# Kernel tuning notes

Hardware: AMD Instinct MI355X
Metric: run time of the kernel (lower is better)

Reference implementation:

```python
import jax, jax.numpy as jnp
import numpy as np

N, H, E, A, T = 50000, 128, 800000, 16, 4


def setup_inputs() -> dict:
    key = jax.random.key(0)
    ks = jax.random.split(key, 12)
    s = 1.0 / np.sqrt(H + A)
    s2 = 1.0 / np.sqrt(H)
    return {
        "h": jax.random.normal(ks[0], (N, H), dtype=jnp.float32),
        "edge_index": jax.random.randint(ks[1], (2, E), 0, N, dtype=jnp.int32),
        "edge_type": jax.random.randint(ks[2], (E,), 0, T, dtype=jnp.int32),
        "edge_attr": jax.random.normal(ks[3], (E, A), dtype=jnp.float32),
        # per-edge-type 2-layer MLP params
        "W1": jax.random.uniform(ks[4], (T, H + A, H), minval=-s, maxval=s, dtype=jnp.float32),
        "b1": jax.random.uniform(ks[5], (T, H), minval=-s, maxval=s, dtype=jnp.float32),
        "W2": jax.random.uniform(ks[6], (T, H, H), minval=-s2, maxval=s2, dtype=jnp.float32),
        "b2": jax.random.uniform(ks[7], (T, H), minval=-s2, maxval=s2, dtype=jnp.float32),
        # GRUCell params (torch layout: [3H, H] with gate order r, z, n)
        "w_ih": jax.random.uniform(ks[8], (3 * H, H), minval=-s2, maxval=s2, dtype=jnp.float32),
        "w_hh": jax.random.uniform(ks[9], (3 * H, H), minval=-s2, maxval=s2, dtype=jnp.float32),
        "b_ih": jax.random.uniform(ks[10], (3 * H,), minval=-s2, maxval=s2, dtype=jnp.float32),
        "b_hh": jax.random.uniform(ks[11], (3 * H,), minval=-s2, maxval=s2, dtype=jnp.float32),
    }


def reference(h, edge_index, edge_type, edge_attr, W1, b1, W2, b2, w_ih, w_hh, b_ih, b_hh):
    src, dst = edge_index[0], edge_index[1]
    h_in = jnp.concatenate([h[src], edge_attr], axis=-1)  # [E, H+A]
    # per-edge-type MLP; loop over small fixed num_edge_types, mask-select
    m = jnp.zeros((h_in.shape[0], H), dtype=h.dtype)
    for t in range(T):
        mt = jax.nn.relu(h_in @ W1[t] + b1[t]) @ W2[t] + b2[t]  # [E, H]
        m = jnp.where((edge_type == t)[:, None], mt, m)
    # scatter-add messages to destination nodes
    msg = jax.ops.segment_sum(m, dst, num_segments=h.shape[0])  # [N, H]
    # GRUCell(msg, h) with torch gate order r, z, n
    gi = msg @ w_ih.T + b_ih  # [N, 3H]
    gh = h @ w_hh.T + b_hh
    i_r, i_z, i_n = jnp.split(gi, 3, axis=-1)
    h_r, h_z, h_n = jnp.split(gh, 3, axis=-1)
    r = jax.nn.sigmoid(i_r + h_r)
    z = jax.nn.sigmoid(i_z + h_z)
    n = jnp.tanh(i_n + r * h_n)
    return (1.0 - z) * n + z * h
```

## Files before the change

kernel.cpp:

```cpp
#include <hip/hip_runtime.h>
#include <stdint.h>

#define Hh 128
#define Aa 16
#define Tt 4
#define K1 144
#define W1T_LD 168
#define WG_LD  136
#define YT_LD  136

typedef float f32x4 __attribute__((ext_vector_type(4)));
typedef __bf16 bf16x8 __attribute__((ext_vector_type(8)));
typedef unsigned short u16x8 __attribute__((ext_vector_type(8)));
typedef unsigned short u16x4 __attribute__((ext_vector_type(4)));
typedef unsigned short u16x2 __attribute__((ext_vector_type(2)));

static __device__ __forceinline__ unsigned short f2bf(float f) {
    unsigned u = __builtin_bit_cast(unsigned, f);
    u += 0x7fffu + ((u >> 16) & 1u);
    return (unsigned short)(u >> 16);
}

static __device__ __forceinline__ float bf2f(unsigned short u) {
    return __builtin_bit_cast(float, (unsigned)u << 16);
}

static __device__ __forceinline__ bf16x8 pack8(const float* __restrict__ x) {
    f32x4 a = *(const f32x4*)x;
    f32x4 b = *(const f32x4*)(x + 4);
    u16x8 t;
    t[0] = f2bf(a[0]); t[1] = f2bf(a[1]); t[2] = f2bf(a[2]); t[3] = f2bf(a[3]);
    t[4] = f2bf(b[0]); t[5] = f2bf(b[1]); t[6] = f2bf(b[2]); t[7] = f2bf(b[3]);
    return __builtin_bit_cast(bf16x8, t);
}

static __device__ __forceinline__ bf16x8 zero_bf8() {
    u16x8 z = {0, 0, 0, 0, 0, 0, 0, 0};
    return __builtin_bit_cast(bf16x8, z);
}

__global__ void cast_kernel(const float* __restrict__ src, unsigned short* __restrict__ dst, int n4) {
    int i = blockIdx.x * blockDim.x + threadIdx.x;
    if (i < n4) {
        f32x4 v = *(const f32x4*)(src + (size_t)i * 4);
        u16x4 o;
        o[0] = f2bf(v[0]); o[1] = f2bf(v[1]); o[2] = f2bf(v[2]); o[3] = f2bf(v[3]);
        *(u16x4*)(dst + (size_t)i * 4) = o;
    }
}

__global__ void hist_kernel(const int* __restrict__ et, const int* __restrict__ eidx,
                            int E, int N, int* __restrict__ cnt, unsigned* __restrict__ rank) {
    for (int i = blockIdx.x * blockDim.x + threadIdx.x; i < E; i += gridDim.x * blockDim.x) {
        int tt = et[i];
        unsigned rD = (unsigned)atomicAdd(&cnt[tt * N + eidx[E + i]], 1);
        unsigned rS = (unsigned)atomicAdd(&cnt[4 * N + tt * N + eidx[i]], 1);
        rank[i] = rD | (rS << 16);
    }
}

__global__ void scanA_kernel(const int* __restrict__ deg2, int nb, int* __restrict__ bsum) {
    __shared__ int red[256];
    const int t = threadIdx.x;
    const int i0 = blockIdx.x * 1024 + t * 4;
    int s = 0;
    #pragma unroll
    for (int j = 0; j < 4; j++) if (i0 + j < nb) s += deg2[i0 + j];
    red[t] = s; __syncthreads();
    for (int d = 128; d > 0; d >>= 1) {
        if (t < d) red[t] += red[t + d];
        __syncthreads();
    }
    if (t == 0) bsum[blockIdx.x] = red[0];
}

__global__ void scanB_kernel(int* __restrict__ bsum, int nblocks,
                             int* __restrict__ rowptrD, int fourN, int E) {
    __shared__ int ts[512];
    const int t = threadIdx.x;
    int v = (t < nblocks) ? bsum[t] : 0;
    ts[t] = v; __syncthreads();
    for (int d = 1; d < 512; d <<= 1) {
        int x = (t >= d) ? ts[t - d] : 0;
        __syncthreads();
        ts[t] += x;
        __syncthreads();
    }
    if (t < nblocks) bsum[t] = ts[t] - v;
    if (t == 0) rowptrD[fourN] = E;
}

__global__ void scanC_kernel(int* __restrict__ cur, int nb, int fourN,
                             const int* __restrict__ bsum, int* __restrict__ rowptrD) {
    __shared__ int ts[256];
    const int t = threadIdx.x;
    const int i0 = blockIdx.x * 1024 + t * 4;
    int v[4];
    #pragma unroll
    for (int j = 0; j < 4; j++) v[j] = (i0 + j < nb) ? cur[i0 + j] : 0;
    int s = v[0] + v[1] + v[2] + v[3];
    ts[t] = s; __syncthreads();
    for (int d = 1; d < 256; d <<= 1) {
        int x = (t >= d) ? ts[t - d] : 0;
        __syncthreads();
        ts[t] += x;
        __syncthreads();
    }
    int run = bsum[blockIdx.x] + ts[t] - s;
    #pragma unroll
    for (int j = 0; j < 4; j++) {
        if (i0 + j < nb) {
            if (i0 + j < fourN) rowptrD[i0 + j] = run;
            cur[i0 + j] = run;
            run += v[j];
        }
    }
}

__global__ void fill2_kernel(const int* __restrict__ et, const int* __restrict__ eidx,
                             int E, int N, const int* __restrict__ binstart,
                             const unsigned* __restrict__ rank, int4* __restrict__ rec) {
    for (int i = blockIdx.x * blockDim.x + threadIdx.x; i < E; i += gridDim.x * blockDim.x) {
        int tt = et[i];
        int d = eidx[E + i], s = eidx[i];
        unsigned r = rank[i];
        int posD = binstart[tt * N + d] + (int)(r & 0xffffu);
        int posS = binstart[4 * N + tt * N + s] + (int)(r >> 16) - E;
        rec[posS] = make_int4(s, i, posD, 0);
    }
}

__global__ __launch_bounds__(512) void l1_kernel(
    const unsigned short* __restrict__ h_bf, const int4* __restrict__ rec,
    const float* __restrict__ eattr, const unsigned short* __restrict__ W1bf,
    const float* __restrict__ b1, const int* __restrict__ rowptrD,
    unsigned short* __restrict__ Yg, int N)
{
    __shared__ unsigned short W1T[128 * W1T_LD];
    __shared__ float b1s[128];
    __shared__ unsigned short yt[8 * 8 * YT_LD];
    const int t = blockIdx.x & 3;
    const int lb = blockIdx.x >> 2;
    const int nbk = gridDim.x >> 2;
    const int tid = threadIdx.x;

    for (int idx = tid; idx < K1 * Hh; idx += 512) {
        int k = idx >> 7, n = idx & 127;
        W1T[n * W1T_LD + k] = W1bf[((size_t)t * K1 + k) * Hh + n];
    }
    for (int idx = tid; idx < (W1T_LD - K1) * Hh; idx += 512) {
        int k = K1 + (idx % (W1T_LD - K1)), n = idx / (W1T_LD - K1);
        W1T[n * W1T_LD + k] = 0;
    }
    if (tid < 128) b1s[tid] = b1[t * Hh + tid];
    __syncthreads();

    const int tstart = rowptrD[t * N];
    const int tend = rowptrD[(t + 1) * N];
    const int cnt = tend - tstart;
    const int ntiles = (cnt + 255) >> 8;
    const int w = tid >> 6, lane = tid & 63;
    const int l15 = lane & 15, q = lane >> 4;
    unsigned short* __restrict__ ytw = yt + w * 8 * YT_LD;

    for (int tile = lb; tile < ntiles; tile += nbk) {
        const int p0 = tstart + tile * 256 + w * 32;
        const int pa = p0 + l15, pb = p0 + 16 + l15;
        const bool va = pa < tend, vb = pb < tend;
        const int4 ra = rec[va ? pa : tstart];
        const int4 rb = rec[vb ? pb : tstart];
        const int sa = ra.x, sb = rb.x;
        const int ea = ra.y, eb = rb.y;
        const int ypa = ra.z, ypb = rb.z;
        const unsigned short* __restrict__ hA = h_bf + (size_t)sa * Hh;
        const unsigned short* __restrict__ hB = h_bf + (size_t)sb * Hh;

        f32x4 acc[8][2];
        #pragma unroll
        for (int mt = 0; mt < 8; mt++) {
            acc[mt][0] = (f32x4){0.f, 0.f, 0.f, 0.f};
            acc[mt][1] = (f32x4){0.f, 0.f, 0.f, 0.f};
        }

        #pragma unroll
        for (int ks = 0; ks < 5; ks++) {
            const int k0 = ks * 32;
            bf16x8 fb_a, fb_b;
            if (ks < 4) {
                fb_a = __builtin_bit_cast(bf16x8, *(const u16x8*)(hA + k0 + q * 8));
                fb_b = __builtin_bit_cast(bf16x8, *(const u16x8*)(hB + k0 + q * 8));
            } else if (q < 2) {
                fb_a = pack8(eattr + (size_t)ea * Aa + q * 8);
                fb_b = pack8(eattr + (size_t)eb * Aa + q * 8);
            } else {
                fb_a = zero_bf8();
                fb_b = zero_bf8();
            }
            #pragma unroll
            for (int mt = 0; mt < 8; mt++) {
                bf16x8 fa = *(const bf16x8*)&W1T[(mt * 16 + l15) * W1T_LD + k0 + q * 8];
                acc[mt][0] = __builtin_amdgcn_mfma_f32_16x16x32_bf16(fa, fb_a, acc[mt][0], 0, 0, 0);
                acc[mt][1] = __builtin_amdgcn_mfma_f32_16x16x32_bf16(fa, fb_b, acc[mt][1], 0, 0, 0);
            }
        }

        #pragma unroll
        for (int g = 0; g < 2; g++) {
            const int yp = g ? ypb : ypa;
            #pragma unroll
            for (int s = 0; s < 2; s++) {
                if ((l15 >> 3) == s) {
                    #pragma unroll
                    for (int mt = 0; mt < 8; mt++) {
                        f32x4 bias = *(const f32x4*)&b1s[mt * 16 + q * 4];
                        u16x4 y;
                        #pragma unroll
                        for (int i = 0; i < 4; i++) {
                            float v = acc[mt][g][i] + bias[i];
                            y[i] = f2bf(v > 0.f ? v : 0.f);
                        }
                        *(u16x4*)&ytw[(l15 & 7) * YT_LD + mt * 16 + q * 4] = y;
                    }
                }
                __asm__ volatile("s_waitcnt lgkmcnt(0)" ::: "memory");
                #pragma unroll
                for (int r0 = 0; r0 < 2; r0++) {
                    const int el = r0 * 4 + q;
                    if (p0 + g * 16 + s * 8 + el < tend) {
                        const int yrow = __shfl(yp, s * 8 + el);
                        u16x8 v = *(const u16x8*)&ytw[el * YT_LD + l15 * 8];
                        *(u16x8*)&Yg[(size_t)yrow * Hh + l15 * 8] = v;
                    }
                }
                __asm__ volatile("s_waitcnt lgkmcnt(0)" ::: "memory");
            }
        }
    }
}

__global__ __launch_bounds__(256) void zgemm_kernel(
    const unsigned short* __restrict__ Yg, const int* __restrict__ rowptrD,
    const unsigned short* __restrict__ W2bf, const float* __restrict__ b2,
    unsigned short* __restrict__ msgb, int N)
{
    __shared__ unsigned short W2T[128 * WG_LD];
    __shared__ float b2s[512];
    __shared__ int cntS[4 * 64];
    const int tid = threadIdx.x;
    const int w = tid >> 6, lane = tid & 63;
    const int l15 = lane & 15, q = lane >> 4;
    const int nodebase = blockIdx.x * 64 + w * 16;
    const int nA = min(nodebase + l15, N - 1);

    if (tid < 512) {
        b2s[tid] = b2[tid];
        b2s[tid + 256] = b2[tid + 256];
    }

    f32x4 acc[8];
    #pragma unroll
    for (int ct = 0; ct < 8; ct++) acc[ct] = (f32x4){0.f, 0.f, 0.f, 0.f};

    for (int t = 0; t < Tt; t++) {
        __syncthreads();
        for (int idx = tid; idx < Hh * Hh; idx += 256) {
            int k = idx >> 7, n = idx & 127;
            W2T[n * WG_LD + k] = W2bf[((size_t)t * Hh + k) * Hh + n];
        }
        __syncthreads();

        const int seg = rowptrD[(size_t)t * N + nA];
        const int len = rowptrD[(size_t)t * N + nA + 1] - seg;
        cntS[w * 64 + t * 16 + l15] = len;

        float asum[32];
        #pragma unroll
        for (int i = 0; i < 32; i++) asum[i] = 0.f;
        for (int j = 0; j < len; j++) {
            const unsigned short* __restrict__ yr = Yg + (size_t)(seg + j) * Hh;
            #pragma unroll
            for (int ks = 0; ks < 4; ks++) {
                u16x8 yv = *(const u16x8*)(yr + ks * 32 + q * 8);
                #pragma unroll
                for (int e = 0; e < 8; e++) asum[ks * 8 + e] += bf2f(yv[e]);
            }
        }

        #pragma unroll
        for (int ks = 0; ks < 4; ks++) {
            u16x8 fr;
            #pragma unroll
            for (int e = 0; e < 8; e++) fr[e] = f2bf(asum[ks * 8 + e]);
            bf16x8 fa = __builtin_bit_cast(bf16x8, fr);
            #pragma unroll
            for (int ct = 0; ct < 8; ct++) {
                bf16x8 fb = *(const bf16x8*)&W2T[(ct * 16 + l15) * WG_LD + ks * 32 + q * 8];
                acc[ct] = __builtin_amdgcn_mfma_f32_16x16x32_bf16(fa, fb, acc[ct], 0, 0, 0);
            }
        }
    }
    __syncthreads();

    #pragma unroll
    for (int ct = 0; ct < 8; ct++) {
        const int c = ct * 16 + l15;
        #pragma unroll
        for (int i = 0; i < 4; i++) {
            int node = nodebase + q * 4 + i;
            if (node < N) {
                float bias = 0.f;
                #pragma unroll
                for (int t = 0; t < Tt; t++)
                    bias += (float)cntS[w * 64 + t * 16 + q * 4 + i] * b2s[t * 128 + c];
                msgb[(size_t)node * Hh + c] = f2bf(acc[ct][i] + bias);
            }
        }
    }
}

__global__ __launch_bounds__(512) void gru_kernel(
    const float* __restrict__ h, const unsigned short* __restrict__ msgb,
    const unsigned short* __restrict__ wihb, const unsigned short* __restrict__ whhb,
    const float* __restrict__ b_ih, const float* __restrict__ b_hh,
    float* __restrict__ out, int N)
{
    __shared__ unsigned short Wg[128 * WG_LD];
    const int tid = threadIdx.x;
    const int w = tid >> 6, lane = tid & 63;
    const int l15 = lane & 15, q = lane >> 4;
    const int nodebase = blockIdx.x * 128 + w * 16;
    const int nA = min(nodebase + l15, N - 1);
    const unsigned short* __restrict__ mrow = msgb + (size_t)nA * Hh;
    const float* __restrict__ hrow = h + (size_t)nA * Hh;

    f32x4 gr[8], gz[8], gin[8], ghn[8];
    #pragma unroll
    for (int ct = 0; ct < 8; ct++) {
        gr[ct] = (f32x4){0.f, 0.f, 0.f, 0.f};
        gz[ct] = (f32x4){0.f, 0.f, 0.f, 0.f};
        gin[ct] = (f32x4){0.f, 0.f, 0.f, 0.f};
        ghn[ct] = (f32x4){0.f, 0.f, 0.f, 0.f};
    }

    auto stage = [&](const unsigned short* __restrict__ Ws, int gate) {
        __syncthreads();
        for (int idx = tid; idx < Hh * Hh / 2; idx += 512) {
            int o = idx >> 6, kk = (idx & 63) * 2;
            *(u16x2*)&Wg[o * WG_LD + kk] =
                *(const u16x2*)&Ws[(size_t)gate * Hh * Hh + o * Hh + kk];
        }
        __syncthreads();
    };
    auto matmulM = [&](f32x4* acc) {
        #pragma unroll
        for (int ks = 0; ks < 4; ks++) {
            bf16x8 fa = __builtin_bit_cast(bf16x8, *(const u16x8*)(mrow + ks * 32 + q * 8));
            #pragma unroll
            for (int ct = 0; ct < 8; ct++) {
                bf16x8 fb = *(const bf16x8*)&Wg[(ct * 16 + l15) * WG_LD + ks * 32 + q * 8];
                acc[ct] = __builtin_amdgcn_mfma_f32_16x16x32_bf16(fa, fb, acc[ct], 0, 0, 0);
            }
        }
    };
    auto matmulH = [&](f32x4* acc) {
        #pragma unroll
        for (int ks = 0; ks < 4; ks++) {
            bf16x8 fa = pack8(hrow + ks * 32 + q * 8);
            #pragma unroll
            for (int ct = 0; ct < 8; ct++) {
                bf16x8 fb = *(const bf16x8*)&Wg[(ct * 16 + l15) * WG_LD + ks * 32 + q * 8];
                acc[ct] = __builtin_amdgcn_mfma_f32_16x16x32_bf16(fa, fb, acc[ct], 0, 0, 0);
            }
        }
    };

    stage(wihb, 0); matmulM(gr);
    stage(whhb, 0); matmulH(gr);
    stage(wihb, 1); matmulM(gz);
    stage(whhb, 1); matmulH(gz);
    stage(wihb, 2); matmulM(gin);
    stage(whhb, 2); matmulH(ghn);

    #pragma unroll
    for (int ct = 0; ct < 8; ct++) {
        int c = ct * 16 + l15;
        float bir = b_ih[c],       bhr = b_hh[c];
        float biz = b_ih[128 + c], bhz = b_hh[128 + c];
        float bin = b_ih[256 + c], bhn = b_hh[256 + c];
        #pragma unroll
        for (int i = 0; i < 4; i++) {
            int node = nodebase + q * 4 + i;
            if (node < N) {
                float rv = 1.f / (1.f + __expf(-(gr[ct][i] + bir + bhr)));
                float zv = 1.f / (1.f + __expf(-(gz[ct][i] + biz + bhz)));
                float npre = gin[ct][i] + bin + rv * (ghn[ct][i] + bhn);
                float e2 = __expf(-2.f * npre);
                float nv = (1.f - e2) / (1.f + e2);
                float hv = h[(size_t)node * Hh + c];
                out[(size_t)node * Hh + c] = (1.f - zv) * nv + zv * hv;
            }
        }
    }
}

static inline size_t align256(size_t x) { return (x + 255) & ~(size_t)255; }

extern "C" void kernel_launch(void* const* d_in, const int* in_sizes, int n_in,
                              void* d_out, int out_size, void* d_ws, size_t ws_size,
                              hipStream_t stream)
{
    const float* h     = (const float*)d_in[0];
    const int*   eidx  = (const int*)d_in[1];
    const int*   et    = (const int*)d_in[2];
    const float* eattr = (const float*)d_in[3];
    const float* W1    = (const float*)d_in[4];
    const float* b1    = (const float*)d_in[5];
    const float* W2    = (const float*)d_in[6];
    const float* b2    = (const float*)d_in[7];
    const float* w_ih  = (const float*)d_in[8];
    const float* w_hh  = (const float*)d_in[9];
    const float* b_ih  = (const float*)d_in[10];
    const float* b_hh  = (const float*)d_in[11];

    const int N = in_sizes[0] / Hh;
    const int E = in_sizes[1] / 2;
    const int nb = 8 * N;
    const int sblocks = (nb + 1023) / 1024;

    char* p = (char*)d_ws;
    unsigned short* msgb = (unsigned short*)p; p += align256((size_t)N * Hh * sizeof(unsigned short));
    unsigned short* Yg = (unsigned short*)p;   p += align256((size_t)E * Hh * sizeof(unsigned short));
    int4* rec = (int4*)p;               p += align256((size_t)E * sizeof(int4));
    unsigned* rank = (unsigned*)p;      p += align256((size_t)E * sizeof(unsigned));
    int* rowptrD = (int*)p;             p += align256(((size_t)4 * N + 1) * sizeof(int));
    int* cur = (int*)p;                 p += align256((size_t)nb * sizeof(int));
    int* bsum = (int*)p;                p += align256(1024 * sizeof(int));
    unsigned short* h_bf = (unsigned short*)p; p += align256((size_t)N * Hh * sizeof(unsigned short));
    unsigned short* W1bf = (unsigned short*)p; p += align256((size_t)Tt * K1 * Hh * sizeof(unsigned short));
    unsigned short* W2bf = (unsigned short*)p; p += align256((size_t)Tt * Hh * Hh * sizeof(unsigned short));
    unsigned short* wihb = (unsigned short*)p; p += align256((size_t)3 * Hh * Hh * sizeof(unsigned short));
    unsigned short* whhb = (unsigned short*)p; p += align256((size_t)3 * Hh * Hh * sizeof(unsigned short));

    hipMemsetAsync(cur, 0, (size_t)nb * sizeof(int), stream);

    {
        int n4h = N * Hh / 4, n41 = Tt * K1 * Hh / 4, n42 = Tt * Hh * Hh / 4;
        int n4g = 3 * Hh * Hh / 4;
        cast_kernel<<<(n4h + 255) / 256, 256, 0, stream>>>(h, h_bf, n4h);
        cast_kernel<<<(n41 + 255) / 256, 256, 0, stream>>>(W1, W1bf, n41);
        cast_kernel<<<(n42 + 255) / 256, 256, 0, stream>>>(W2, W2bf, n42);
        cast_kernel<<<(n4g + 255) / 256, 256, 0, stream>>>(w_ih, wihb, n4g);
        cast_kernel<<<(n4g + 255) / 256, 256, 0, stream>>>(w_hh, whhb, n4g);
    }

    hist_kernel<<<1024, 256, 0, stream>>>(et, eidx, E, N, cur, rank);
    scanA_kernel<<<sblocks, 256, 0, stream>>>(cur, nb, bsum);
    scanB_kernel<<<1, 512, 0, stream>>>(bsum, sblocks, rowptrD, 4 * N, E);
    scanC_kernel<<<sblocks, 256, 0, stream>>>(cur, nb, 4 * N, bsum, rowptrD);
    fill2_kernel<<<1024, 256, 0, stream>>>(et, eidx, E, N, cur, rank, rec);

    l1_kernel<<<1024, 512, 0, stream>>>(h_bf, rec, eattr, W1bf, b1, rowptrD, Yg, N);
    zgemm_kernel<<<(N + 63) / 64, 256, 0, stream>>>(Yg, rowptrD, W2bf, b2, msgb, N);

    int gblocks = (N + 127) / 128;
    gru_kernel<<<gblocks, 512, 0, stream>>>(h, msgb, wihb, whhb, b_ih, b_hh, (float*)d_out, N);
}
```

Measured before the change: 491.0 us.

## Merge cast launches, drop LDS staging in l1 epilogue, preload GRU fragments

Merges the five bf16 cast launches into a single kernel. In the layer-1 kernel, the output is written straight to global memory from the MFMA accumulators instead of being staged through shared memory with shuffles, and the W1 transpose load is vectorized. The kernel also gets an occupancy hint, and the grid size is doubled. The GRU kernel now preloads msg and h fragments once (reading the bf16 copy of h) and reuses them across the six gate matmuls, with wider weight staging loads. The direct l1 stores are narrower 8-byte scattered writes, which may coalesce less well than the old 16-byte row stores.

```diff
diff --git a/kernel.cpp b/kernel.cpp
--- a/kernel.cpp
+++ b/kernel.cpp
@@ -7,7 +7,6 @@
 #define K1 144
 #define W1T_LD 168
 #define WG_LD  136
-#define YT_LD  136
 
 typedef float f32x4 __attribute__((ext_vector_type(4)));
 typedef __bf16 bf16x8 __attribute__((ext_vector_type(8)));
@@ -39,14 +38,27 @@
     return __builtin_bit_cast(bf16x8, z);
 }
 
-__global__ void cast_kernel(const float* __restrict__ src, unsigned short* __restrict__ dst, int n4) {
+__global__ void cast_all_kernel(
+    const float* __restrict__ h, const float* __restrict__ W1,
+    const float* __restrict__ W2, const float* __restrict__ wih,
+    const float* __restrict__ whh,
+    unsigned short* __restrict__ h_bf, unsigned short* __restrict__ W1bf,
+    unsigned short* __restrict__ W2bf, unsigned short* __restrict__ wihb,
+    unsigned short* __restrict__ whhb,
+    int n0, int n1, int n2, int n3, int n4)
+{
     int i = blockIdx.x * blockDim.x + threadIdx.x;
-    if (i < n4) {
-        f32x4 v = *(const f32x4*)(src + (size_t)i * 4);
-        u16x4 o;
-        o[0] = f2bf(v[0]); o[1] = f2bf(v[1]); o[2] = f2bf(v[2]); o[3] = f2bf(v[3]);
-        *(u16x4*)(dst + (size_t)i * 4) = o;
-    }
+    if (i >= n4) return;
+    const float* s; unsigned short* d; int off;
+    if (i < n0)      { s = h;   d = h_bf; off = i; }
+    else if (i < n1) { s = W1;  d = W1bf; off = i - n0; }
+    else if (i < n2) { s = W2;  d = W2bf; off = i - n1; }
+    else if (i < n3) { s = wih; d = wihb; off = i - n2; }
+    else             { s = whh; d = whhb; off = i - n3; }
+    f32x4 v = *(const f32x4*)(s + (size_t)off * 4);
+    u16x4 o;
+    o[0] = f2bf(v[0]); o[1] = f2bf(v[1]); o[2] = f2bf(v[2]); o[3] = f2bf(v[3]);
+    *(u16x4*)(d + (size_t)off * 4) = o;
 }
 
 __global__ void hist_kernel(const int* __restrict__ et, const int* __restrict__ eidx,
@@ -130,7 +142,7 @@
     }
 }
 
-__global__ __launch_bounds__(512) void l1_kernel(
+__global__ __launch_bounds__(512, 6) void l1_kernel(
     const unsigned short* __restrict__ h_bf, const int4* __restrict__ rec,
     const float* __restrict__ eattr, const unsigned short* __restrict__ W1bf,
     const float* __restrict__ b1, const int* __restrict__ rowptrD,
@@ -138,19 +150,21 @@
 {
     __shared__ unsigned short W1T[128 * W1T_LD];
     __shared__ float b1s[128];
-    __shared__ unsigned short yt[8 * 8 * YT_LD];
     const int t = blockIdx.x & 3;
     const int lb = blockIdx.x >> 2;
     const int nbk = gridDim.x >> 2;
     const int tid = threadIdx.x;
 
-    for (int idx = tid; idx < K1 * Hh; idx += 512) {
-        int k = idx >> 7, n = idx & 127;
-        W1T[n * W1T_LD + k] = W1bf[((size_t)t * K1 + k) * Hh + n];
-    }
-    for (int idx = tid; idx < (W1T_LD - K1) * Hh; idx += 512) {
-        int k = K1 + (idx % (W1T_LD - K1)), n = idx / (W1T_LD - K1);
-        W1T[n * W1T_LD + k] = 0;
+    for (int idx = tid; idx < (K1 * Hh) / 8; idx += 512) {
+        int k = idx >> 4, n0 = (idx & 15) * 8;
+        u16x8 v = *(const u16x8*)&W1bf[((size_t)t * K1 + k) * Hh + n0];
+        #pragma unroll
+        for (int j = 0; j < 8; j++) W1T[(n0 + j) * W1T_LD + k] = v[j];
+    }
+    for (int idx = tid; idx < Hh * 3; idx += 512) {
+        int n = idx / 3, c = (idx % 3) * 8;
+        u16x8 z = {0, 0, 0, 0, 0, 0, 0, 0};
+        *(u16x8*)&W1T[n * W1T_LD + K1 + c] = z;
     }
     if (tid < 128) b1s[tid] = b1[t * Hh + tid];
     __syncthreads();
@@ -161,7 +175,6 @@
     const int ntiles = (cnt + 255) >> 8;
     const int w = tid >> 6, lane = tid & 63;
     const int l15 = lane & 15, q = lane >> 4;
-    unsigned short* __restrict__ ytw = yt + w * 8 * YT_LD;
 
     for (int tile = lb; tile < ntiles; tile += nbk) {
         const int p0 = tstart + tile * 256 + w * 32;
@@ -206,33 +219,19 @@
 
         #pragma unroll
         for (int g = 0; g < 2; g++) {
-            const int yp = g ? ypb : ypa;
-            #pragma unroll
-            for (int s = 0; s < 2; s++) {
-                if ((l15 >> 3) == s) {
+            if (g ? vb : va) {
+                unsigned short* __restrict__ o = Yg + (size_t)(g ? ypb : ypa) * Hh + q * 4;
+                #pragma unroll
+                for (int mt = 0; mt < 8; mt++) {
+                    f32x4 bias = *(const f32x4*)&b1s[mt * 16 + q * 4];
+                    u16x4 y;
                     #pragma unroll
-                    for (int mt = 0; mt < 8; mt++) {
-                        f32x4 bias = *(const f32x4*)&b1s[mt * 16 + q * 4];
-                        u16x4 y;
-                        #pragma unroll
-                        for (int i = 0; i < 4; i++) {
-                            float v = acc[mt][g][i] + bias[i];
-                            y[i] = f2bf(v > 0.f ? v : 0.f);
-                        }
-                        *(u16x4*)&ytw[(l15 & 7) * YT_LD + mt * 16 + q * 4] = y;
+                    for (int i = 0; i < 4; i++) {
+                        float v = acc[mt][g][i] + bias[i];
+                        y[i] = f2bf(v > 0.f ? v : 0.f);
                     }
+                    *(u16x4*)(o + mt * 16) = y;
                 }
-                __asm__ volatile("s_waitcnt lgkmcnt(0)" ::: "memory");
-                #pragma unroll
-                for (int r0 = 0; r0 < 2; r0++) {
-                    const int el = r0 * 4 + q;
-                    if (p0 + g * 16 + s * 8 + el < tend) {
-                        const int yrow = __shfl(yp, s * 8 + el);
-                        u16x8 v = *(const u16x8*)&ytw[el * YT_LD + l15 * 8];
-                        *(u16x8*)&Yg[(size_t)yrow * Hh + l15 * 8] = v;
-                    }
-                }
-                __asm__ volatile("s_waitcnt lgkmcnt(0)" ::: "memory");
             }
         }
     }
@@ -319,7 +318,8 @@
 }
 
 __global__ __launch_bounds__(512) void gru_kernel(
-    const float* __restrict__ h, const unsigned short* __restrict__ msgb,
+    const float* __restrict__ h, const unsigned short* __restrict__ h_bf,
+    const unsigned short* __restrict__ msgb,
     const unsigned short* __restrict__ wihb, const unsigned short* __restrict__ whhb,
     const float* __restrict__ b_ih, const float* __restrict__ b_hh,
     float* __restrict__ out, int N)
@@ -330,8 +330,13 @@
     const int l15 = lane & 15, q = lane >> 4;
     const int nodebase = blockIdx.x * 128 + w * 16;
     const int nA = min(nodebase + l15, N - 1);
-    const unsigned short* __restrict__ mrow = msgb + (size_t)nA * Hh;
-    const float* __restrict__ hrow = h + (size_t)nA * Hh;
+
+    bf16x8 fm[4], fh[4];
+    #pragma unroll
+    for (int ks = 0; ks < 4; ks++) {
+        fm[ks] = __builtin_bit_cast(bf16x8, *(const u16x8*)(msgb + (size_t)nA * Hh + ks * 32 + q * 8));
+        fh[ks] = __builtin_bit_cast(bf16x8, *(const u16x8*)(h_bf + (size_t)nA * Hh + ks * 32 + q * 8));
+    }
 
     f32x4 gr[8], gz[8], gin[8], ghn[8];
     #pragma unroll
@@ -344,42 +349,30 @@
 
     auto stage = [&](const unsigned short* __restrict__ Ws, int gate) {
         __syncthreads();
-        for (int idx = tid; idx < Hh * Hh / 2; idx += 512) {
-            int o = idx >> 6, kk = (idx & 63) * 2;
-            *(u16x2*)&Wg[o * WG_LD + kk] =
-                *(const u16x2*)&Ws[(size_t)gate * Hh * Hh + o * Hh + kk];
+        for (int idx = tid; idx < (Hh * Hh) / 8; idx += 512) {
+            int o = idx >> 4, k8 = (idx & 15) * 8;
+            *(u16x8*)&Wg[o * WG_LD + k8] =
+                *(const u16x8*)&Ws[(size_t)gate * Hh * Hh + o * Hh + k8];
         }
         __syncthreads();
     };
-    auto matmulM = [&](f32x4* acc) {
+    auto matmul = [&](f32x4* acc, const bf16x8* fa) {
         #pragma unroll
         for (int ks = 0; ks < 4; ks++) {
-            bf16x8 fa = __builtin_bit_cast(bf16x8, *(const u16x8*)(mrow + ks * 32 + q * 8));
             #pragma unroll
             for (int ct = 0; ct < 8; ct++) {
                 bf16x8 fb = *(const bf16x8*)&Wg[(ct * 16 + l15) * WG_LD + ks * 32 + q * 8];
-                acc[ct] = __builtin_amdgcn_mfma_f32_16x16x32_bf16(fa, fb, acc[ct], 0, 0, 0);
+                acc[ct] = __builtin_amdgcn_mfma_f32_16x16x32_bf16(fa[ks], fb, acc[ct], 0, 0, 0);
             }
         }
     };
-    auto matmulH = [&](f32x4* acc) {
-        #pragma unroll
-        for (int ks = 0; ks < 4; ks++) {
-            bf16x8 fa = pack8(hrow + ks * 32 + q * 8);
-            #pragma unroll
-            for (int ct = 0; ct < 8; ct++) {
-                bf16x8 fb = *(const bf16x8*)&Wg[(ct * 16 + l15) * WG_LD + ks * 32 + q * 8];
-                acc[ct] = __builtin_amdgcn_mfma_f32_16x16x32_bf16(fa, fb, acc[ct], 0, 0, 0);
-            }
-        }
-    };
-
-    stage(wihb, 0); matmulM(gr);
-    stage(whhb, 0); matmulH(gr);
-    stage(wihb, 1); matmulM(gz);
-    stage(whhb, 1); matmulH(gz);
-    stage(wihb, 2); matmulM(gin);
-    stage(whhb, 2); matmulH(ghn);
+
+    stage(wihb, 0); matmul(gr, fm);
+    stage(whhb, 0); matmul(gr, fh);
+    stage(wihb, 1); matmul(gz, fm);
+    stage(whhb, 1); matmul(gz, fh);
+    stage(wihb, 2); matmul(gin, fm);
+    stage(whhb, 2); matmul(ghn, fh);
 
     #pragma unroll
     for (int ct = 0; ct < 8; ct++) {
@@ -446,11 +439,9 @@
     {
         int n4h = N * Hh / 4, n41 = Tt * K1 * Hh / 4, n42 = Tt * Hh * Hh / 4;
         int n4g = 3 * Hh * Hh / 4;
-        cast_kernel<<<(n4h + 255) / 256, 256, 0, stream>>>(h, h_bf, n4h);
-        cast_kernel<<<(n41 + 255) / 256, 256, 0, stream>>>(W1, W1bf, n41);
-        cast_kernel<<<(n42 + 255) / 256, 256, 0, stream>>>(W2, W2bf, n42);
-        cast_kernel<<<(n4g + 255) / 256, 256, 0, stream>>>(w_ih, wihb, n4g);
-        cast_kernel<<<(n4g + 255) / 256, 256, 0, stream>>>(w_hh, whhb, n4g);
+        int c0 = n4h, c1 = c0 + n41, c2 = c1 + n42, c3 = c2 + n4g, c4 = c3 + n4g;
+        cast_all_kernel<<<(c4 + 255) / 256, 256, 0, stream>>>(
+            h, W1, W2, w_ih, w_hh, h_bf, W1bf, W2bf, wihb, whhb, c0, c1, c2, c3, c4);
     }
 
     hist_kernel<<<1024, 256, 0, stream>>>(et, eidx, E, N, cur, rank);
@@ -459,9 +450,9 @@
     scanC_kernel<<<sblocks, 256, 0, stream>>>(cur, nb, 4 * N, bsum, rowptrD);
     fill2_kernel<<<1024, 256, 0, stream>>>(et, eidx, E, N, cur, rank, rec);
 
-    l1_kernel<<<1024, 512, 0, stream>>>(h_bf, rec, eattr, W1bf, b1, rowptrD, Yg, N);
+    l1_kernel<<<2048, 512, 0, stream>>>(h_bf, rec, eattr, W1bf, b1, rowptrD, Yg, N);
     zgemm_kernel<<<(N + 63) / 64, 256, 0, stream>>>(Yg, rowptrD, W2bf, b2, msgb, N);
 
     int gblocks = (N + 127) / 128;
-    gru_kernel<<<gblocks, 512, 0, stream>>>(h, msgb, wihb, whhb, b_ih, b_hh, (float*)d_out, N);
-}
+    gru_kernel<<<gblocks, 512, 0, stream>>>(h, h_bf, msgb, wihb, whhb, b_ih, b_hh, (float*)d_out, N);
+}
```

Measured after the change: 1.159 ms. 136% more time.
